# Kernel tuning notes

Measured on AMD Instinct MI355X. Metric: run time of the kernel, lower is better.

The kernel has to match this reference:

```python
import jax, jax.numpy as jnp
import numpy as np

NEG_SLOPE = 0.1
BN_EPS = 1e-5

def lrelu(z):
    return jax.nn.leaky_relu(z, NEG_SLOPE)

def conv1d(x, w, b):
    # x: [B,C,L], w: [O,I,K], 'same' padding for K=3
    y = jax.lax.conv_general_dilated(x, w, (1,), [(1, 1)], dimension_numbers=('NCH', 'OIH', 'NCH'))
    return y + b[None, :, None]

def batchnorm_train(x, g, be):
    # training-mode BatchNorm1d over (B, L) per channel; x: [B,C,L]
    m = x.mean(axis=(0, 2), keepdims=True)
    v = x.var(axis=(0, 2), keepdims=True)
    return g[None, :, None] * (x - m) * jax.lax.rsqrt(v + BN_EPS) + be[None, :, None]

def setup_inputs() -> dict:
    key = jax.random.key(0)
    ks = jax.random.split(key, 16)
    L, B, E = 100, 32, 512
    F, K, M, H, DEC = 256, 3, 128, 512, 512
    D = F + 2  # cnn feats + 2 coord dims
    s = 0.02
    inp = {
        'x': jax.random.normal(ks[0], (L, B, E), jnp.float32),
        'h': jax.random.normal(ks[1], (B, H), jnp.float32),
        'cw1': jax.random.normal(ks[2], (F, E, K), jnp.float32) * s,
        'cb1': jnp.zeros((F,), jnp.float32),
        'g1': jnp.ones((F,), jnp.float32), 'be1': jnp.zeros((F,), jnp.float32),
        'cw2': jax.random.normal(ks[3], (F, F, K), jnp.float32) * s,
        'cb2': jnp.zeros((F,), jnp.float32),
        'g2': jnp.ones((F,), jnp.float32), 'be2': jnp.zeros((F,), jnp.float32),
        'cw3': jax.random.normal(ks[4], (F, F, K), jnp.float32) * s,
        'cb3': jnp.zeros((F,), jnp.float32),
        'g3': jnp.ones((F,), jnp.float32), 'be3': jnp.zeros((F,), jnp.float32),
        'cw4': jax.random.normal(ks[5], (F, F, K), jnp.float32) * s,
        'cb4': jnp.zeros((F,), jnp.float32),
        'g4': jnp.ones((F,), jnp.float32), 'be4': jnp.zeros((F,), jnp.float32),
        'W1': jax.random.normal(ks[6], (2 * D + H, M), jnp.float32) * s,
        'b1': jnp.zeros((M,), jnp.float32),
        'W2': jax.random.normal(ks[7], (M, M), jnp.float32) * s,
        'b2': jnp.zeros((M,), jnp.float32),
        'W3': jax.random.normal(ks[8], (M, M), jnp.float32) * s,
        'b3': jnp.zeros((M,), jnp.float32),
        'W4': jax.random.normal(ks[9], (M, M), jnp.float32) * s,
        'b4': jnp.zeros((M,), jnp.float32),
        'F1': jax.random.normal(ks[10], (M, M), jnp.float32) * s,
        'fb1': jnp.zeros((M,), jnp.float32),
        'F2': jax.random.normal(ks[11], (M, DEC), jnp.float32) * s,
        'fb2': jnp.zeros((DEC,), jnp.float32),
    }
    return inp

def reference(x, h, cw1, cb1, g1, be1, cw2, cb2, g2, be2, cw3, cb3, g3, be3,
              cw4, cb4, g4, be4, W1, b1, W2, b2, W3, b3, W4, b4, F1, fb1, F2, fb2):
    # x: [L,B,E] -> [B,E,L]
    xc = jnp.transpose(x, (1, 2, 0))
    for cw, cb, g, be in ((cw1, cb1, g1, be1), (cw2, cb2, g2, be2),
                          (cw3, cb3, g3, be3), (cw4, cb4, g4, be4)):
        xc = batchnorm_train(lrelu(conv1d(xc, cw, cb)), g, be)
    xc = jnp.transpose(xc, (0, 2, 1))  # [B,L,F]
    B, L, _ = xc.shape
    # coordinate tensor: cvt_coord(i, L) = [(i/sqrt(L)-2)/2, (i%sqrt(L)-2)/2]
    i = jnp.arange(L, dtype=jnp.float32)
    sL = jnp.sqrt(jnp.float32(L))
    coord = jnp.stack([(i / sL - 2.0) / 2.0, (jnp.mod(i, sL) - 2.0) / 2.0], axis=-1)
    xf = jnp.concatenate([xc, jnp.broadcast_to(coord, (B, L, 2))], axis=-1)  # [B,L,D]
    D = xf.shape[-1]
    # pair[b,i,j] = [xf[b,j], xf[b,i], h[b]]; split W1 to avoid materializing concat
    Wa, Wb, Wc = W1[:D], W1[D:2 * D], W1[2 * D:]
    A = xf @ Wa                              # contribution of x_j, [B,L,M]
    C = xf @ Wb + (h @ Wc + b1)[:, None, :]  # contribution of x_i and h, [B,L,M]
    g = lrelu(C[:, :, None, :] + A[:, None, :, :])  # [B,L,L,M]
    g = lrelu(g @ W2 + b2)
    g = lrelu(g @ W3 + b3)
    g = lrelu(g @ W4 + b4)
    s = g.sum(axis=(1, 2))  # sum-pool over all L*L pairs -> [B,M]
    out = lrelu(lrelu(s @ F1 + fb1) @ F2 + fb2)  # [B,dec_hid]
    return out
```

## Files before the change

kernel.cpp:

```cpp
#include <hip/hip_runtime.h>
#include <hip/hip_bf16.h>
#include <stdint.h>
#include <stddef.h>

#define NEG 0.1f

typedef __attribute__((ext_vector_type(8))) short short8;
typedef __attribute__((ext_vector_type(16))) float floatx16;

__device__ __forceinline__ unsigned f2bf(float f) {
  union { float f; unsigned u; } v; v.f = f;
  unsigned r = v.u + 0x7FFFu + ((v.u >> 16) & 1u);
  return r >> 16;
}
__device__ __forceinline__ unsigned pk2bf(float a, float b) {
  __hip_bfloat162 hh = __float22bfloat162_rn(make_float2(a, b));
  union { __hip_bfloat162 h; unsigned u; } v; v.h = hh; return v.u;
}
__device__ __forceinline__ float bits2f(unsigned u) {
  union { unsigned u; float f; } v; v.u = u; return v.f;
}

__global__ void k_prep(const float* __restrict__ cw1, const float* __restrict__ cw2,
                       const float* __restrict__ cw3, const float* __restrict__ cw4,
                       unsigned short* __restrict__ wt1, unsigned short* __restrict__ wt2,
                       unsigned short* __restrict__ wt3, unsigned short* __restrict__ wt4,
                       const float* __restrict__ W1, unsigned short* __restrict__ wab,
                       const float* __restrict__ W2, const float* __restrict__ W3,
                       const float* __restrict__ W4, unsigned short* __restrict__ wmlp,
                       const float* __restrict__ h, float* __restrict__ hc) {
  __shared__ float tile[64 * 65];
  int bid = blockIdx.x, tid = threadIdx.x;
  if (bid < 1280) {
    int z = bid;
    int E; const float* cw; unsigned short* wt;
    if (z < 512) { E = 512; cw = cw1; wt = wt1; }
    else {
      int q = (z - 512) >> 8; E = 256;
      cw = (q == 0) ? cw2 : ((q == 1) ? cw3 : cw4);
      wt = (q == 0) ? wt2 : ((q == 1) ? wt3 : wt4);
      z = (z - 512) & 255;
    }
    int idx = z * 256 + tid;
    int f = idx / E, e = idx - f * E;
    const float* s = cw + (size_t)idx * 3;
    unsigned short* d = wt + (size_t)f * 3 * E + e;
    d[0] = (unsigned short)f2bf(s[0]);
    d[E] = (unsigned short)f2bf(s[1]);
    d[2 * E] = (unsigned short)f2bf(s[2]);
  } else if (bid < 1304) {
    int tw = bid - 1280;
    int half = tw / 12, rem = tw % 12, dt = rem >> 1, nt = rem & 1;
    int c = tid & 63, rq = tid >> 6;
#pragma unroll
    for (int it = 0; it < 16; ++it) {
      int r = rq + it * 4;
      int kp = dt * 64 + r;
      float v = 0.f;
      if (kp < 258) v = W1[(size_t)(half * 258 + kp) * 128 + nt * 64 + c];
      tile[r * 65 + c] = v;
    }
    __syncthreads();
#pragma unroll
    for (int it = 0; it < 16; ++it) {
      int r2 = rq + it * 4;
      wab[(size_t)(half * 128 + nt * 64 + r2) * 384 + dt * 64 + c] =
          (unsigned short)f2bf(tile[c * 65 + r2]);
    }
  } else if (bid < 1496) {
    int i2 = (bid - 1304) * 256 + tid;
    int n = i2 & 127, k = (i2 >> 7) & 127, zz = i2 >> 14;
    const float* W = (zz == 0) ? W2 : ((zz == 1) ? W3 : W4);
    float v = W[k * 128 + n];
    int w = n >> 5, l = ((k >> 3) & 1) * 32 + (n & 31), kk = k >> 4, j = k & 7;
    int i = (((zz * 4 + w) * 8 + kk) << 9) | (l << 3) | j;
    wmlp[i] = (unsigned short)f2bf(v);
  } else {
    int t = bid - 1496;
    int b = t >> 2, seg = t & 3;
    int m = tid & 127, sub = tid >> 7;
    int k0 = seg * 128 + sub * 64;
    const float* hr = h + b * 512 + k0;
    const float* Wc = W1 + (size_t)(516 + k0) * 128 + m;
    float a0 = 0.f, a1 = 0.f, a2 = 0.f, a3 = 0.f, a4 = 0.f, a5 = 0.f, a6 = 0.f, a7 = 0.f;
#pragma unroll
    for (int k = 0; k < 64; k += 8) {
      a0 += hr[k + 0] * Wc[(size_t)(k + 0) * 128];
      a1 += hr[k + 1] * Wc[(size_t)(k + 1) * 128];
      a2 += hr[k + 2] * Wc[(size_t)(k + 2) * 128];
      a3 += hr[k + 3] * Wc[(size_t)(k + 3) * 128];
      a4 += hr[k + 4] * Wc[(size_t)(k + 4) * 128];
      a5 += hr[k + 5] * Wc[(size_t)(k + 5) * 128];
      a6 += hr[k + 6] * Wc[(size_t)(k + 6) * 128];
      a7 += hr[k + 7] * Wc[(size_t)(k + 7) * 128];
    }
    float s = ((a0 + a1) + (a2 + a3)) + ((a4 + a5) + (a6 + a7));
    atomicAdd(&hc[b * 128 + m], s);
  }
}

__global__ __launch_bounds__(256, 2) void k_conv(
    const float* __restrict__ zin, const float* __restrict__ bnin,
    const float* __restrict__ gamv, const float* __restrict__ betv,
    const unsigned short* __restrict__ wt, const float* __restrict__ cb,
    float* __restrict__ zout, float* __restrict__ bnout, int E, int xmode) {
  extern __shared__ unsigned short smem[];
  const int SL = (E == 512) ? 520 : 264;
  unsigned short* slab = smem;
  unsigned short* Bs = smem + 34 * SL;
  const int K = 3 * E, NC = K >> 6, NCH = NC >> 1;
  const int esh = (E == 512) ? 9 : 8;
  int tid = threadIdx.x;
  int lane = tid & 63, wave = tid >> 6;
  int khalf = wave >> 1, cwave = wave & 1;
  int r0 = blockIdx.x * 32, ct = blockIdx.y;
  int i32 = lane & 31;
  int koff = (lane >> 5) << 3;

  int lrow = (r0 + i32) % 100;
  bool vks0 = (lrow >= 1), vks2 = (lrow <= 98);

  if (xmode) {
    for (int s = wave; s < 34; s += 4) {
      int m = r0 - 1 + s; m = min(max(m, 0), 3199);
      int b = m / 100, l = m - b * 100;
      size_t base = (size_t)(l * 32 + b) * 512;
#pragma unroll
      for (int cc = 0; cc < 2; ++cc) {
        int ch = cc * 256 + lane * 4;
        float4 v = *(const float4*)(zin + base + ch);
        uint2 p; p.x = pk2bf(v.x, v.y); p.y = pk2bf(v.z, v.w);
        *(uint2*)(&slab[s * SL + ch]) = p;
      }
    }
  } else {
    const float inv = 1.f / 3200.f;
    float sc[4], sh[4];
#pragma unroll
    for (int q = 0; q < 4; ++q) {
      int ch = lane * 4 + q;
      float mme = bnin[ch] * inv;
      float var = bnin[256 + ch] * inv - mme * mme;
      sc[q] = gamv[ch] * rsqrtf(var + 1e-5f);
      sh[q] = betv[ch] - mme * sc[q];
    }
    for (int s = wave; s < 34; s += 4) {
      int m = r0 - 1 + s; m = min(max(m, 0), 3199);
      float4 v = *(const float4*)(zin + (size_t)m * 256 + lane * 4);
      uint2 p;
      p.x = pk2bf(v.x * sc[0] + sh[0], v.y * sc[1] + sh[1]);
      p.y = pk2bf(v.z * sc[2] + sh[2], v.w * sc[3] + sh[3]);
      *(uint2*)(&slab[s * SL + lane * 4]) = p;
    }
  }

  floatx16 acc;
#pragma unroll
  for (int q = 0; q < 16; ++q) acc[q] = 0.f;

  int t128 = tid & 127;
  int brow = t128 >> 1, bhalf = (t128 & 1) * 32;
  const unsigned short* wrow = wt + (size_t)(ct * 64 + brow) * K + khalf * NCH * 64 + bhalf;
  uint4 pre[4];
#pragma unroll
  for (int t = 0; t < 4; ++t) pre[t] = *(const uint4*)(wrow + t * 8);

  for (int c = 0; c < NCH; ++c) {
    unsigned short* Bc = Bs + (khalf * 2 + (c & 1)) * (64 * 72);
#pragma unroll
    for (int t = 0; t < 4; ++t)
      *(uint4*)(&Bc[brow * 72 + bhalf + t * 8]) = pre[t];
    __syncthreads();
    if (c + 1 < NCH) {
#pragma unroll
      for (int t = 0; t < 4; ++t)
        pre[t] = *(const uint4*)(wrow + (c + 1) * 64 + t * 8);
    }
    int cg = khalf * NCH + c;
    int ks = (cg << 6) >> esh;
    int ebase = (cg << 6) & (E - 1);
    bool v = (ks == 0) ? vks0 : ((ks == 2) ? vks2 : true);
    int srow = i32 + ks;
#pragma unroll
    for (int kk = 0; kk < 4; ++kk) {
      short8 a = {};
      if (v) a = *(const short8*)(&slab[srow * SL + ebase + kk * 16 + koff]);
      short8 b8 = *(const short8*)(&Bc[(cwave * 32 + i32) * 72 + kk * 16 + koff]);
      acc = __builtin_amdgcn_mfma_f32_32x32x16_bf16(a, b8, acc, 0, 0, 0);
    }
  }

  __syncthreads();
  float* scr = (float*)smem;
  if (khalf == 1) {
#pragma unroll
    for (int reg = 0; reg < 16; ++reg) {
      int rowp = (reg & 3) + 8 * (reg >> 2) + 4 * (lane >> 5);
      scr[cwave * 1024 + rowp * 32 + i32] = acc[reg];
    }
  }
  __syncthreads();
  if (khalf == 0) {
    int f = ct * 64 + cwave * 32 + i32;
    float bias = cb[f];
    float s1 = 0.f, s2 = 0.f;
#pragma unroll
    for (int reg = 0; reg < 16; ++reg) {
      int rowp = (reg & 3) + 8 * (reg >> 2) + 4 * (lane >> 5);
      int m = r0 + rowp;
      float v = acc[reg] + scr[cwave * 1024 + rowp * 32 + i32] + bias;
      v = fmaxf(v, NEG * v);
      zout[(size_t)m * 256 + f] = v;
      s1 += v; s2 += v * v;
    }
    s1 += __shfl_xor(s1, 32, 64);
    s2 += __shfl_xor(s2, 32, 64);
    if (lane < 32) { atomicAdd(&bnout[f], s1); atomicAdd(&bnout[256 + f], s2); }
  }
}

__global__ __launch_bounds__(128, 2) void k_ac(
    const float* __restrict__ zin, const float* __restrict__ bnin,
    const float* __restrict__ gamv, const float* __restrict__ betv,
    const unsigned short* __restrict__ wab, const float* __restrict__ hc,
    const float* __restrict__ b1v,
    unsigned short* __restrict__ Abf, unsigned short* __restrict__ Cbf) {
  __shared__ unsigned short slab[32 * 328];
  __shared__ unsigned short Bs[2 * 64 * 72];
  int tid = threadIdx.x;
  int lane = tid & 63, wave = tid >> 6;
  int r0 = blockIdx.x * 32, ct = blockIdx.y;
  int i32 = lane & 31;
  int koff = (lane >> 5) << 3;
  const float inv = 1.f / 3200.f;

  {
    float sc[4], sh[4];
#pragma unroll
    for (int q = 0; q < 4; ++q) {
      int ch = lane * 4 + q;
      float mme = bnin[ch] * inv;
      float var = bnin[256 + ch] * inv - mme * mme;
      sc[q] = gamv[ch] * rsqrtf(var + 1e-5f);
      sh[q] = betv[ch] - mme * sc[q];
    }
    for (int s = wave; s < 32; s += 2) {
      int m = r0 + s;
      float4 v = *(const float4*)(zin + (size_t)m * 256 + lane * 4);
      uint2 p;
      p.x = pk2bf(v.x * sc[0] + sh[0], v.y * sc[1] + sh[1]);
      p.y = pk2bf(v.z * sc[2] + sh[2], v.w * sc[3] + sh[3]);
      *(uint2*)(&slab[s * 328 + lane * 4]) = p;
    }
    if (wave == 0) {
      int s = i32, half = (lane >> 5) * 32;
      int m = r0 + s, l = m % 100;
      float c0 = ((float)l * 0.1f - 2.0f) * 0.5f;
      float c1 = ((float)(l % 10) - 2.0f) * 0.5f;
#pragma unroll
      for (int seg = 0; seg < 4; ++seg) {
        uint4 z4; z4.x = z4.y = z4.z = z4.w = 0u;
        if (half == 0 && seg == 0) z4.x = pk2bf(c0, c1);
        *(uint4*)(&slab[s * 328 + 256 + half + seg * 8]) = z4;
      }
    }
  }

  floatx16 acc;
#pragma unroll
  for (int q = 0; q < 16; ++q) acc[q] = 0.f;

  int brow = tid >> 1, bhalf = (tid & 1) * 32;
  uint4 pre[4];
#pragma unroll
  for (int t = 0; t < 4; ++t)
    pre[t] = *(const uint4*)(wab + (size_t)(ct * 64 + brow) * 384 + bhalf + t * 8);

  for (int c = 0; c < 5; ++c) {
    unsigned short* Bc = Bs + (c & 1) * (64 * 72);
#pragma unroll
    for (int t = 0; t < 4; ++t)
      *(uint4*)(&Bc[brow * 72 + bhalf + t * 8]) = pre[t];
    __syncthreads();
    if (c + 1 < 5) {
#pragma unroll
      for (int t = 0; t < 4; ++t)
        pre[t] = *(const uint4*)(wab + (size_t)(ct * 64 + brow) * 384 + (c + 1) * 64 + bhalf + t * 8);
    }
#pragma unroll
    for (int kk = 0; kk < 4; ++kk) {
      short8 a = *(const short8*)(&slab[i32 * 328 + c * 64 + kk * 16 + koff]);
      short8 b8 = *(const short8*)(&Bc[(wave * 32 + i32) * 72 + kk * 16 + koff]);
      acc = __builtin_amdgcn_mfma_f32_32x32x16_bf16(a, b8, acc, 0, 0, 0);
    }
  }

  int n = ct * 64 + wave * 32 + i32;
#pragma unroll
  for (int reg = 0; reg < 16; ++reg) {
    int rowp = (reg & 3) + 8 * (reg >> 2) + 4 * (lane >> 5);
    int m = r0 + rowp;
    float v = acc[reg];
    if (ct < 2) {
      Abf[(size_t)m * 128 + n] = (unsigned short)f2bf(v);
    } else {
      int b = m / 100;
      int nc = n - 128;
      Cbf[(size_t)m * 128 + nc] =
          (unsigned short)f2bf(v + hc[b * 128 + nc] + b1v[nc]);
    }
  }
}

__device__ __forceinline__ void mlp_layer(const int z, const unsigned short* wlds,
                                          const float* bias_lds, const int lane,
                                          const int h, const short8 (&gin)[8],
                                          short8 (&gout)[8]) {
#pragma unroll
  for (int a = 0; a < 4; ++a) {
    floatx16 acc;
#pragma unroll
    for (int q = 0; q < 16; ++q) acc[q] = 0.f;
#pragma unroll
    for (int kk = 0; kk < 8; ++kk) {
      short8 wf = *(const short8*)(wlds + (((z * 4 + a) * 8 + kk) << 9) + lane * 8);
      acc = __builtin_amdgcn_mfma_f32_32x32x16_bf16(wf, gin[kk], acc, 0, 0, 0);
    }
#pragma unroll
    for (int qg = 0; qg < 4; ++qg) {
      float4 bb = *(const float4*)(bias_lds + z * 128 + a * 32 + qg * 8 + h * 4);
      float v0 = acc[qg * 4 + 0] + bb.x;
      float v1 = acc[qg * 4 + 1] + bb.y;
      float v2 = acc[qg * 4 + 2] + bb.z;
      float v3 = acc[qg * 4 + 3] + bb.w;
      acc[qg * 4 + 0] = fmaxf(v0, NEG * v0);
      acc[qg * 4 + 1] = fmaxf(v1, NEG * v1);
      acc[qg * 4 + 2] = fmaxf(v2, NEG * v2);
      acc[qg * 4 + 3] = fmaxf(v3, NEG * v3);
    }
#pragma unroll
    for (int c = 0; c < 2; ++c) {
      unsigned X0 = pk2bf(acc[8 * c + 0], acc[8 * c + 1]);
      unsigned X1 = pk2bf(acc[8 * c + 2], acc[8 * c + 3]);
      unsigned Y0 = pk2bf(acc[8 * c + 4], acc[8 * c + 5]);
      unsigned Y1 = pk2bf(acc[8 * c + 6], acc[8 * c + 7]);
      auto p0 = __builtin_amdgcn_permlane32_swap(X0, Y0, false, false);
      auto p1 = __builtin_amdgcn_permlane32_swap(X1, Y1, false, false);
      union { unsigned w[4]; short8 s; } uu;
      uu.w[0] = (unsigned)p0[0]; uu.w[1] = (unsigned)p1[0];
      uu.w[2] = (unsigned)p0[1]; uu.w[3] = (unsigned)p1[1];
      gout[2 * a + c] = uu.s;
    }
  }
}

__global__ __launch_bounds__(1024, 4) void k_mlp(
    const unsigned short* __restrict__ Abf, const unsigned short* __restrict__ Cbf,
    const unsigned short* __restrict__ wmlp, const float* __restrict__ b2,
    const float* __restrict__ b3, const float* __restrict__ b4,
    float* __restrict__ sout) {
  extern __shared__ unsigned short wsm[];
  float* bias_lds = (float*)(wsm + 49152);
  int tid = threadIdx.x, lane = tid & 63, wave = tid >> 6;
  int ln31 = lane & 31, h = lane >> 5;

  {
    const uint4* s4 = (const uint4*)wmlp;
    uint4* d4 = (uint4*)wsm;
#pragma unroll
    for (int i = 0; i < 6; ++i) d4[tid + i * 1024] = s4[tid + i * 1024];
    if (tid < 256) bias_lds[tid] = (tid < 128) ? b2[tid] : b3[tid - 128];
  }
  float b4v[4];
#pragma unroll
  for (int a = 0; a < 4; ++a) b4v[a] = b4[a * 32 + ln31];
  __syncthreads();

  int slot = blockIdx.x * 16 + wave;
  for (int it = 0; it < 3; ++it) {
    int u = it * 4096 + slot;
    if (u >= 10016) break;
    int b = u / 313, lu = u - b * 313;
    int r = lu * 32 + ln31;
    int rc = min(r, 9999);
    int i = rc / 100, j = rc - i * 100;
    const unsigned short* Crow = Cbf + (size_t)(b * 100 + i) * 128 + h * 8;
    const unsigned short* Arow = Abf + (size_t)(b * 100 + j) * 128 + h * 8;

    short8 ga[8], gb[8];
#pragma unroll
    for (int kk = 0; kk < 8; ++kk) {
      uint4 c4 = *(const uint4*)(Crow + kk * 16);
      uint4 a4 = *(const uint4*)(Arow + kk * 16);
      unsigned cw[4] = {c4.x, c4.y, c4.z, c4.w};
      unsigned aw[4] = {a4.x, a4.y, a4.z, a4.w};
      unsigned ow[4];
#pragma unroll
      for (int q = 0; q < 4; ++q) {
        float x0 = bits2f(cw[q] << 16) + bits2f(aw[q] << 16);
        float x1 = bits2f(cw[q] & 0xFFFF0000u) + bits2f(aw[q] & 0xFFFF0000u);
        x0 = fmaxf(x0, NEG * x0);
        x1 = fmaxf(x1, NEG * x1);
        ow[q] = pk2bf(x0, x1);
      }
      union { unsigned w[4]; short8 s; } uu;
      uu.w[0] = ow[0]; uu.w[1] = ow[1]; uu.w[2] = ow[2]; uu.w[3] = ow[3];
      ga[kk] = uu.s;
    }

    mlp_layer(0, wsm, bias_lds, lane, h, ga, gb);
    mlp_layer(1, wsm, bias_lds, lane, h, gb, ga);

#pragma unroll
    for (int a = 0; a < 4; ++a) {
      floatx16 acc;
#pragma unroll
      for (int q = 0; q < 16; ++q) acc[q] = 0.f;
#pragma unroll
      for (int kk = 0; kk < 8; ++kk) {
        short8 wf = *(const short8*)(wsm + (((8 + a) * 8 + kk) << 9) + lane * 8);
        acc = __builtin_amdgcn_mfma_f32_32x32x16_bf16(ga[kk], wf, acc, 0, 0, 0);
      }
      float s = 0.f;
#pragma unroll
      for (int reg = 0; reg < 16; ++reg) {
        int rowp = (reg & 3) + 8 * (reg >> 2) + 4 * h;
        float v = acc[reg] + b4v[a];
        v = fmaxf(v, NEG * v);
        s += (lu * 32 + rowp < 10000) ? v : 0.f;
      }
      s += __shfl_xor(s, 32, 64);
      if (lane < 32) atomicAdd(&sout[b * 128 + a * 32 + ln31], s);
    }
  }
}

__global__ void k_final(const float* __restrict__ s, const float* __restrict__ F1,
                        const float* __restrict__ fb1, const float* __restrict__ F2,
                        const float* __restrict__ fb2, float* __restrict__ out) {
  __shared__ float sl[128], t1[128];
  int b = blockIdx.x, t = threadIdx.x;
  if (t < 128) sl[t] = s[b * 128 + t];
  __syncthreads();
  if (t < 128) {
    float a = fb1[t];
    for (int k = 0; k < 128; ++k) a += sl[k] * F1[k * 128 + t];
    t1[t] = fmaxf(a, NEG * a);
  }
  __syncthreads();
  for (int o = t; o < 512; o += 256) {
    float a = fb2[o];
    for (int k = 0; k < 128; ++k) a += t1[k] * F2[k * 512 + o];
    out[b * 512 + o] = fmaxf(a, NEG * a);
  }
}

extern "C" void kernel_launch(void* const* d_in, const int* in_sizes, int n_in,
                              void* d_out, int out_size, void* d_ws, size_t ws_size,
                              hipStream_t stream) {
  const float* x   = (const float*)d_in[0];
  const float* h   = (const float*)d_in[1];
  const float* cw1 = (const float*)d_in[2];
  const float* cb1 = (const float*)d_in[3];
  const float* g1  = (const float*)d_in[4];
  const float* be1 = (const float*)d_in[5];
  const float* cw2 = (const float*)d_in[6];
  const float* cb2 = (const float*)d_in[7];
  const float* g2  = (const float*)d_in[8];
  const float* be2 = (const float*)d_in[9];
  const float* cw3 = (const float*)d_in[10];
  const float* cb3 = (const float*)d_in[11];
  const float* g3  = (const float*)d_in[12];
  const float* be3 = (const float*)d_in[13];
  const float* cw4 = (const float*)d_in[14];
  const float* cb4 = (const float*)d_in[15];
  const float* g4  = (const float*)d_in[16];
  const float* be4 = (const float*)d_in[17];
  const float* W1  = (const float*)d_in[18];
  const float* b1  = (const float*)d_in[19];
  const float* W2  = (const float*)d_in[20];
  const float* b2  = (const float*)d_in[21];
  const float* W3  = (const float*)d_in[22];
  const float* b3  = (const float*)d_in[23];
  const float* W4  = (const float*)d_in[24];
  const float* b4  = (const float*)d_in[25];
  const float* F1  = (const float*)d_in[26];
  const float* fb1 = (const float*)d_in[27];
  const float* F2  = (const float*)d_in[28];
  const float* fb2 = (const float*)d_in[29];

  char* ws = (char*)d_ws;
  float* bn0  = (float*)(ws + 0);
  float* bn1  = (float*)(ws + 2048);
  float* bn2  = (float*)(ws + 4096);
  float* bn3  = (float*)(ws + 6144);
  float* sbuf = (float*)(ws + 8192);
  float* hc   = (float*)(ws + 24576);
  float* za   = (float*)(ws + 40960);
  float* zb   = (float*)(ws + 3317760);
  unsigned short* wt1  = (unsigned short*)(ws + 6594560);
  unsigned short* wt2  = (unsigned short*)(ws + 7380992);
  unsigned short* wt3  = (unsigned short*)(ws + 7774208);
  unsigned short* wt4  = (unsigned short*)(ws + 8167424);
  unsigned short* wab  = (unsigned short*)(ws + 8560640);
  unsigned short* wmlp = (unsigned short*)(ws + 8757248);
  unsigned short* Abf  = (unsigned short*)(ws + 8855552);
  unsigned short* Cbf  = (unsigned short*)(ws + 9674752);

  hipMemsetAsync(d_ws, 0, 40960, stream);

  k_prep<<<1624, 256, 0, stream>>>(cw1, cw2, cw3, cw4, wt1, wt2, wt3, wt4,
                                   W1, wab, W2, W3, W4, wmlp, h, hc);

  const int lds1 = (34 * 520 + 4 * 64 * 72) * 2;
  const int lds2 = (34 * 264 + 4 * 64 * 72) * 2;
  k_conv<<<dim3(100, 4), 256, lds1, stream>>>(x,  nullptr, nullptr, nullptr, wt1, cb1, za, bn0, 512, 1);
  k_conv<<<dim3(100, 4), 256, lds2, stream>>>(za, bn0, g1, be1, wt2, cb2, zb, bn1, 256, 0);
  k_conv<<<dim3(100, 4), 256, lds2, stream>>>(zb, bn1, g2, be2, wt3, cb3, za, bn2, 256, 0);
  k_conv<<<dim3(100, 4), 256, lds2, stream>>>(za, bn2, g3, be3, wt4, cb4, zb, bn3, 256, 0);

  k_ac<<<dim3(100, 4), 128, 0, stream>>>(zb, bn3, g4, be4, wab, hc, b1, Abf, Cbf);

  const int ldsm = 49152 * 2 + 256 * 4;
  k_mlp<<<256, 1024, ldsm, stream>>>(Abf, Cbf, wmlp, b2, b3, b4, sbuf);
  k_final<<<32, 256, 0, stream>>>(sbuf, F1, fb1, F2, fb2, (float*)d_out);
}
```

Before: 280.8 us.

## Pre-swizzle conv weights into MFMA fragment layout and split K across waves

Conv and A/C projection weights are now stored during prep in MFMA-fragment order, so each wave loads B operands straight from global memory without staging them through LDS. The conv and k_ac kernels switch to 32-column tiles with K split four ways across waves and a reduction through LDS, doubling the grid and raising occupancy. Other changes: the memset is folded into the prep kernel, the hc atomics become a block reduction, biases seed the MLP accumulators, and the pair-pooling kernel skips row masking except on the tail tile. The K-split adds an LDS reduction, and weights are now read uncached by each block.

```diff
diff --git a/kernel.cpp b/kernel.cpp
--- a/kernel.cpp
+++ b/kernel.cpp
@@ -21,15 +21,17 @@
   union { unsigned u; float f; } v; v.u = u; return v.f;
 }
 
+
 __global__ void k_prep(const float* __restrict__ cw1, const float* __restrict__ cw2,
                        const float* __restrict__ cw3, const float* __restrict__ cw4,
                        unsigned short* __restrict__ wt1, unsigned short* __restrict__ wt2,
                        unsigned short* __restrict__ wt3, unsigned short* __restrict__ wt4,
-                       const float* __restrict__ W1, unsigned short* __restrict__ wab,
+                       const float* __restrict__ W1, unsigned short* __restrict__ wabf,
                        const float* __restrict__ W2, const float* __restrict__ W3,
                        const float* __restrict__ W4, unsigned short* __restrict__ wmlp,
-                       const float* __restrict__ h, float* __restrict__ hc) {
-  __shared__ float tile[64 * 65];
+                       const float* __restrict__ h, float* __restrict__ hc,
+                       float* __restrict__ zmem) {
+  __shared__ float tile[256];
   int bid = blockIdx.x, tid = threadIdx.x;
   if (bid < 1280) {
     int z = bid;
@@ -41,31 +43,34 @@
       wt = (q == 0) ? wt2 : ((q == 1) ? wt3 : wt4);
       z = (z - 512) & 255;
     }
+    int NCw = (3 * E) >> 6;
     int idx = z * 256 + tid;
     int f = idx / E, e = idx - f * E;
     const float* s = cw + (size_t)idx * 3;
-    unsigned short* d = wt + (size_t)f * 3 * E + e;
-    d[0] = (unsigned short)f2bf(s[0]);
-    d[E] = (unsigned short)f2bf(s[1]);
-    d[2 * E] = (unsigned short)f2bf(s[2]);
+    int ct = f >> 5, i32 = f & 31;
+#pragma unroll
+    for (int ks = 0; ks < 3; ++ks) {
+      int kcol = ks * E + e;
+      int cg = kcol >> 6, kk = (kcol >> 4) & 3, hh = (kcol >> 3) & 1, j = kcol & 7;
+      wt[(size_t)((((ct * NCw + cg) * 4 + kk) * 2 + hh) * 32 + i32) * 8 + j] =
+          (unsigned short)f2bf(s[ks]);
+    }
   } else if (bid < 1304) {
     int tw = bid - 1280;
     int half = tw / 12, rem = tw % 12, dt = rem >> 1, nt = rem & 1;
     int c = tid & 63, rq = tid >> 6;
-#pragma unroll
-    for (int it = 0; it < 16; ++it) {
-      int r = rq + it * 4;
-      int kp = dt * 64 + r;
-      float v = 0.f;
-      if (kp < 258) v = W1[(size_t)(half * 258 + kp) * 128 + nt * 64 + c];
-      tile[r * 65 + c] = v;
-    }
-    __syncthreads();
+    int n = half * 128 + nt * 64 + c;
+    int ct = n >> 5, i32 = n & 31;
 #pragma unroll
     for (int it = 0; it < 16; ++it) {
       int r2 = rq + it * 4;
-      wab[(size_t)(half * 128 + nt * 64 + r2) * 384 + dt * 64 + c] =
-          (unsigned short)f2bf(tile[c * 65 + r2]);
+      int kp = dt * 64 + r2;
+      if (kp < 320) {
+        float v = (kp < 258) ? W1[(size_t)(half * 258 + kp) * 128 + nt * 64 + c] : 0.f;
+        int cg = kp >> 6, kk = (kp >> 4) & 3, hh = (kp >> 3) & 1, j = kp & 7;
+        wabf[(size_t)((((ct * 5 + cg) * 4 + kk) * 2 + hh) * 32 + i32) * 8 + j] =
+            (unsigned short)f2bf(v);
+      }
     }
   } else if (bid < 1496) {
     int i2 = (bid - 1304) * 256 + tid;
@@ -75,16 +80,14 @@
     int w = n >> 5, l = ((k >> 3) & 1) * 32 + (n & 31), kk = k >> 4, j = k & 7;
     int i = (((zz * 4 + w) * 8 + kk) << 9) | (l << 3) | j;
     wmlp[i] = (unsigned short)f2bf(v);
-  } else {
-    int t = bid - 1496;
-    int b = t >> 2, seg = t & 3;
-    int m = tid & 127, sub = tid >> 7;
-    int k0 = seg * 128 + sub * 64;
-    const float* hr = h + b * 512 + k0;
-    const float* Wc = W1 + (size_t)(516 + k0) * 128 + m;
+  } else if (bid < 1528) {
+    int b = bid - 1496;
+    int m = tid & 127, kh = tid >> 7;
+    const float* hr = h + b * 512 + kh * 256;
+    const float* Wc = W1 + (size_t)(516 + kh * 256) * 128 + m;
     float a0 = 0.f, a1 = 0.f, a2 = 0.f, a3 = 0.f, a4 = 0.f, a5 = 0.f, a6 = 0.f, a7 = 0.f;
 #pragma unroll
-    for (int k = 0; k < 64; k += 8) {
+    for (int k = 0; k < 256; k += 8) {
       a0 += hr[k + 0] * Wc[(size_t)(k + 0) * 128];
       a1 += hr[k + 1] * Wc[(size_t)(k + 1) * 128];
       a2 += hr[k + 2] * Wc[(size_t)(k + 2) * 128];
@@ -95,27 +98,30 @@
       a7 += hr[k + 7] * Wc[(size_t)(k + 7) * 128];
     }
     float s = ((a0 + a1) + (a2 + a3)) + ((a4 + a5) + (a6 + a7));
-    atomicAdd(&hc[b * 128 + m], s);
-  }
-}
-
-__global__ __launch_bounds__(256, 2) void k_conv(
+    tile[tid] = s;
+    __syncthreads();
+    if (kh == 0) hc[b * 128 + m] = tile[m] + tile[128 + m];
+  } else {
+    int i = (bid - 1528) * 256 + tid;
+    zmem[i] = 0.f;
+  }
+}
+
+__global__ __launch_bounds__(256, 4) void k_conv(
     const float* __restrict__ zin, const float* __restrict__ bnin,
     const float* __restrict__ gamv, const float* __restrict__ betv,
-    const unsigned short* __restrict__ wt, const float* __restrict__ cb,
+    const unsigned short* __restrict__ wtf, const float* __restrict__ cb,
     float* __restrict__ zout, float* __restrict__ bnout, int E, int xmode) {
   extern __shared__ unsigned short smem[];
   const int SL = (E == 512) ? 520 : 264;
   unsigned short* slab = smem;
-  unsigned short* Bs = smem + 34 * SL;
-  const int K = 3 * E, NC = K >> 6, NCH = NC >> 1;
+  const int NC = (3 * E) >> 6, NCQ = NC >> 2;
   const int esh = (E == 512) ? 9 : 8;
   int tid = threadIdx.x;
   int lane = tid & 63, wave = tid >> 6;
-  int khalf = wave >> 1, cwave = wave & 1;
-  int r0 = blockIdx.x * 32, ct = blockIdx.y;
-  int i32 = lane & 31;
-  int koff = (lane >> 5) << 3;
+  int bid = blockIdx.x;
+  int r0 = (bid % 100) * 32, ct = bid / 100;
+  int i32 = lane & 31, h = lane >> 5;
 
   int lrow = (r0 + i32) % 100;
   bool vks0 = (lrow >= 1), vks2 = (lrow <= 98);
@@ -153,30 +159,28 @@
       *(uint2*)(&slab[s * SL + lane * 4]) = p;
     }
   }
+  __syncthreads();
 
   floatx16 acc;
 #pragma unroll
   for (int q = 0; q < 16; ++q) acc[q] = 0.f;
 
-  int t128 = tid & 127;
-  int brow = t128 >> 1, bhalf = (t128 & 1) * 32;
-  const unsigned short* wrow = wt + (size_t)(ct * 64 + brow) * K + khalf * NCH * 64 + bhalf;
-  uint4 pre[4];
-#pragma unroll
-  for (int t = 0; t < 4; ++t) pre[t] = *(const uint4*)(wrow + t * 8);
-
-  for (int c = 0; c < NCH; ++c) {
-    unsigned short* Bc = Bs + (khalf * 2 + (c & 1)) * (64 * 72);
-#pragma unroll
-    for (int t = 0; t < 4; ++t)
-      *(uint4*)(&Bc[brow * 72 + bhalf + t * 8]) = pre[t];
-    __syncthreads();
-    if (c + 1 < NCH) {
-#pragma unroll
-      for (int t = 0; t < 4; ++t)
-        pre[t] = *(const uint4*)(wrow + (c + 1) * 64 + t * 8);
-    }
-    int cg = khalf * NCH + c;
+  int cg0 = wave * NCQ;
+  const unsigned short* wp = wtf + (size_t)((ct * NC + cg0) * 8 + h) * 256 + i32 * 8;
+  short8 bpre[4];
+#pragma unroll
+  for (int kk = 0; kk < 4; ++kk) bpre[kk] = *(const short8*)(wp + kk * 512);
+
+  for (int c = 0; c < NCQ; ++c) {
+    short8 bcur[4];
+#pragma unroll
+    for (int kk = 0; kk < 4; ++kk) bcur[kk] = bpre[kk];
+    if (c + 1 < NCQ) {
+      wp += 2048;
+#pragma unroll
+      for (int kk = 0; kk < 4; ++kk) bpre[kk] = *(const short8*)(wp + kk * 512);
+    }
+    int cg = cg0 + c;
     int ks = (cg << 6) >> esh;
     int ebase = (cg << 6) & (E - 1);
     bool v = (ks == 0) ? vks0 : ((ks == 2) ? vks2 : true);
@@ -184,31 +188,31 @@
 #pragma unroll
     for (int kk = 0; kk < 4; ++kk) {
       short8 a = {};
-      if (v) a = *(const short8*)(&slab[srow * SL + ebase + kk * 16 + koff]);
-      short8 b8 = *(const short8*)(&Bc[(cwave * 32 + i32) * 72 + kk * 16 + koff]);
-      acc = __builtin_amdgcn_mfma_f32_32x32x16_bf16(a, b8, acc, 0, 0, 0);
+      if (v) a = *(const short8*)(&slab[srow * SL + ebase + kk * 16 + h * 8]);
+      acc = __builtin_amdgcn_mfma_f32_32x32x16_bf16(a, bcur[kk], acc, 0, 0, 0);
     }
   }
 
   __syncthreads();
   float* scr = (float*)smem;
-  if (khalf == 1) {
+  if (wave) {
 #pragma unroll
     for (int reg = 0; reg < 16; ++reg) {
-      int rowp = (reg & 3) + 8 * (reg >> 2) + 4 * (lane >> 5);
-      scr[cwave * 1024 + rowp * 32 + i32] = acc[reg];
-    }
-  }
-  __syncthreads();
-  if (khalf == 0) {
-    int f = ct * 64 + cwave * 32 + i32;
+      int rowp = (reg & 3) + 8 * (reg >> 2) + 4 * h;
+      scr[(wave - 1) * 1024 + rowp * 32 + i32] = acc[reg];
+    }
+  }
+  __syncthreads();
+  if (wave == 0) {
+    int f = ct * 32 + i32;
     float bias = cb[f];
     float s1 = 0.f, s2 = 0.f;
 #pragma unroll
     for (int reg = 0; reg < 16; ++reg) {
-      int rowp = (reg & 3) + 8 * (reg >> 2) + 4 * (lane >> 5);
+      int rowp = (reg & 3) + 8 * (reg >> 2) + 4 * h;
       int m = r0 + rowp;
-      float v = acc[reg] + scr[cwave * 1024 + rowp * 32 + i32] + bias;
+      float v = acc[reg] + scr[rowp * 32 + i32] + scr[1024 + rowp * 32 + i32]
+              + scr[2048 + rowp * 32 + i32] + bias;
       v = fmaxf(v, NEG * v);
       zout[(size_t)m * 256 + f] = v;
       s1 += v; s2 += v * v;
@@ -219,19 +223,19 @@
   }
 }
 
-__global__ __launch_bounds__(128, 2) void k_ac(
+__global__ __launch_bounds__(256, 4) void k_ac(
     const float* __restrict__ zin, const float* __restrict__ bnin,
     const float* __restrict__ gamv, const float* __restrict__ betv,
-    const unsigned short* __restrict__ wab, const float* __restrict__ hc,
+    const unsigned short* __restrict__ wabf, const float* __restrict__ hc,
     const float* __restrict__ b1v,
     unsigned short* __restrict__ Abf, unsigned short* __restrict__ Cbf) {
-  __shared__ unsigned short slab[32 * 328];
-  __shared__ unsigned short Bs[2 * 64 * 72];
+  extern __shared__ unsigned short smem[];
+  unsigned short* slab = smem;
   int tid = threadIdx.x;
   int lane = tid & 63, wave = tid >> 6;
-  int r0 = blockIdx.x * 32, ct = blockIdx.y;
-  int i32 = lane & 31;
-  int koff = (lane >> 5) << 3;
+  int bid = blockIdx.x;
+  int r0 = (bid % 100) * 32, ct = bid / 100;
+  int i32 = lane & 31, h = lane >> 5;
   const float inv = 1.f / 3200.f;
 
   {
@@ -244,7 +248,7 @@
       sc[q] = gamv[ch] * rsqrtf(var + 1e-5f);
       sh[q] = betv[ch] - mme * sc[q];
     }
-    for (int s = wave; s < 32; s += 2) {
+    for (int s = wave; s < 32; s += 4) {
       int m = r0 + s;
       float4 v = *(const float4*)(zin + (size_t)m * 256 + lane * 4);
       uint2 p;
@@ -253,7 +257,7 @@
       *(uint2*)(&slab[s * 328 + lane * 4]) = p;
     }
     if (wave == 0) {
-      int s = i32, half = (lane >> 5) * 32;
+      int s = i32, half = h * 32;
       int m = r0 + s, l = m % 100;
       float c0 = ((float)l * 0.1f - 2.0f) * 0.5f;
       float c1 = ((float)(l % 10) - 2.0f) * 0.5f;
@@ -265,49 +269,52 @@
       }
     }
   }
+  __syncthreads();
 
   floatx16 acc;
 #pragma unroll
   for (int q = 0; q < 16; ++q) acc[q] = 0.f;
 
-  int brow = tid >> 1, bhalf = (tid & 1) * 32;
-  uint4 pre[4];
-#pragma unroll
-  for (int t = 0; t < 4; ++t)
-    pre[t] = *(const uint4*)(wab + (size_t)(ct * 64 + brow) * 384 + bhalf + t * 8);
-
-  for (int c = 0; c < 5; ++c) {
-    unsigned short* Bc = Bs + (c & 1) * (64 * 72);
-#pragma unroll
-    for (int t = 0; t < 4; ++t)
-      *(uint4*)(&Bc[brow * 72 + bhalf + t * 8]) = pre[t];
-    __syncthreads();
-    if (c + 1 < 5) {
-#pragma unroll
-      for (int t = 0; t < 4; ++t)
-        pre[t] = *(const uint4*)(wab + (size_t)(ct * 64 + brow) * 384 + (c + 1) * 64 + bhalf + t * 8);
-    }
-#pragma unroll
-    for (int kk = 0; kk < 4; ++kk) {
-      short8 a = *(const short8*)(&slab[i32 * 328 + c * 64 + kk * 16 + koff]);
-      short8 b8 = *(const short8*)(&Bc[(wave * 32 + i32) * 72 + kk * 16 + koff]);
-      acc = __builtin_amdgcn_mfma_f32_32x32x16_bf16(a, b8, acc, 0, 0, 0);
-    }
-  }
-
-  int n = ct * 64 + wave * 32 + i32;
-#pragma unroll
-  for (int reg = 0; reg < 16; ++reg) {
-    int rowp = (reg & 3) + 8 * (reg >> 2) + 4 * (lane >> 5);
-    int m = r0 + rowp;
-    float v = acc[reg];
-    if (ct < 2) {
-      Abf[(size_t)m * 128 + n] = (unsigned short)f2bf(v);
-    } else {
-      int b = m / 100;
-      int nc = n - 128;
-      Cbf[(size_t)m * 128 + nc] =
-          (unsigned short)f2bf(v + hc[b * 128 + nc] + b1v[nc]);
+#pragma unroll
+  for (int cc = 0; cc < 2; ++cc) {
+    int cg = wave + cc * 4;
+    if (cg <= 4) {
+      const unsigned short* wp = wabf + (size_t)((ct * 5 + cg) * 8 + h) * 256 + i32 * 8;
+#pragma unroll
+      for (int kk = 0; kk < 4; ++kk) {
+        short8 a = *(const short8*)(&slab[i32 * 328 + cg * 64 + kk * 16 + h * 8]);
+        short8 b8 = *(const short8*)(wp + kk * 512);
+        acc = __builtin_amdgcn_mfma_f32_32x32x16_bf16(a, b8, acc, 0, 0, 0);
+      }
+    }
+  }
+
+  __syncthreads();
+  float* scr = (float*)smem;
+  if (wave) {
+#pragma unroll
+    for (int reg = 0; reg < 16; ++reg) {
+      int rowp = (reg & 3) + 8 * (reg >> 2) + 4 * h;
+      scr[(wave - 1) * 1024 + rowp * 32 + i32] = acc[reg];
+    }
+  }
+  __syncthreads();
+  if (wave == 0) {
+    int n = ct * 32 + i32;
+#pragma unroll
+    for (int reg = 0; reg < 16; ++reg) {
+      int rowp = (reg & 3) + 8 * (reg >> 2) + 4 * h;
+      int m = r0 + rowp;
+      float v = acc[reg] + scr[rowp * 32 + i32] + scr[1024 + rowp * 32 + i32]
+              + scr[2048 + rowp * 32 + i32];
+      if (ct < 4) {
+        Abf[(size_t)m * 128 + n] = (unsigned short)f2bf(v);
+      } else {
+        int b = m / 100;
+        int nc = n - 128;
+        Cbf[(size_t)m * 128 + nc] =
+            (unsigned short)f2bf(v + hc[b * 128 + nc] + b1v[nc]);
+      }
     }
   }
 }
@@ -320,23 +327,20 @@
   for (int a = 0; a < 4; ++a) {
     floatx16 acc;
 #pragma unroll
-    for (int q = 0; q < 16; ++q) acc[q] = 0.f;
+    for (int qg = 0; qg < 4; ++qg) {
+      float4 bb = *(const float4*)(bias_lds + z * 128 + a * 32 + qg * 8 + h * 4);
+      acc[qg * 4 + 0] = bb.x; acc[qg * 4 + 1] = bb.y;
+      acc[qg * 4 + 2] = bb.z; acc[qg * 4 + 3] = bb.w;
+    }
 #pragma unroll
     for (int kk = 0; kk < 8; ++kk) {
       short8 wf = *(const short8*)(wlds + (((z * 4 + a) * 8 + kk) << 9) + lane * 8);
       acc = __builtin_amdgcn_mfma_f32_32x32x16_bf16(wf, gin[kk], acc, 0, 0, 0);
     }
 #pragma unroll
-    for (int qg = 0; qg < 4; ++qg) {
-      float4 bb = *(const float4*)(bias_lds + z * 128 + a * 32 + qg * 8 + h * 4);
-      float v0 = acc[qg * 4 + 0] + bb.x;
-      float v1 = acc[qg * 4 + 1] + bb.y;
-      float v2 = acc[qg * 4 + 2] + bb.z;
-      float v3 = acc[qg * 4 + 3] + bb.w;
-      acc[qg * 4 + 0] = fmaxf(v0, NEG * v0);
-      acc[qg * 4 + 1] = fmaxf(v1, NEG * v1);
-      acc[qg * 4 + 2] = fmaxf(v2, NEG * v2);
-      acc[qg * 4 + 3] = fmaxf(v3, NEG * v3);
+    for (int q = 0; q < 16; ++q) {
+      float v = acc[q];
+      acc[q] = fmaxf(v, NEG * v);
     }
 #pragma unroll
     for (int c = 0; c < 2; ++c) {
@@ -381,8 +385,9 @@
     int u = it * 4096 + slot;
     if (u >= 10016) break;
     int b = u / 313, lu = u - b * 313;
+    bool tail = (lu == 312);
     int r = lu * 32 + ln31;
-    int rc = min(r, 9999);
+    int rc = tail ? min(r, 9999) : r;
     int i = rc / 100, j = rc - i * 100;
     const unsigned short* Crow = Cbf + (size_t)(b * 100 + i) * 128 + h * 8;
     const unsigned short* Arow = Abf + (size_t)(b * 100 + j) * 128 + h * 8;
@@ -414,20 +419,29 @@
 #pragma unroll
     for (int a = 0; a < 4; ++a) {
       floatx16 acc;
-#pragma unroll
-      for (int q = 0; q < 16; ++q) acc[q] = 0.f;
+      float binit = b4v[a];
+#pragma unroll
+      for (int q = 0; q < 16; ++q) acc[q] = binit;
 #pragma unroll
       for (int kk = 0; kk < 8; ++kk) {
         short8 wf = *(const short8*)(wsm + (((8 + a) * 8 + kk) << 9) + lane * 8);
         acc = __builtin_amdgcn_mfma_f32_32x32x16_bf16(ga[kk], wf, acc, 0, 0, 0);
       }
       float s = 0.f;
-#pragma unroll
-      for (int reg = 0; reg < 16; ++reg) {
-        int rowp = (reg & 3) + 8 * (reg >> 2) + 4 * h;
-        float v = acc[reg] + b4v[a];
-        v = fmaxf(v, NEG * v);
-        s += (lu * 32 + rowp < 10000) ? v : 0.f;
+      if (!tail) {
+#pragma unroll
+        for (int reg = 0; reg < 16; ++reg) {
+          float v = acc[reg];
+          s += fmaxf(v, NEG * v);
+        }
+      } else {
+#pragma unroll
+        for (int reg = 0; reg < 16; ++reg) {
+          int rowp = (reg & 3) + 8 * (reg >> 2) + 4 * h;
+          float v = acc[reg];
+          v = fmaxf(v, NEG * v);
+          s += (lu * 32 + rowp < 10000) ? v : 0.f;
+        }
       }
       s += __shfl_xor(s, 32, 64);
       if (lane < 32) atomicAdd(&sout[b * 128 + a * 32 + ln31], s);
@@ -490,6 +504,7 @@
   const float* fb2 = (const float*)d_in[29];
 
   char* ws = (char*)d_ws;
+  float* zmem = (float*)(ws + 0);
   float* bn0  = (float*)(ws + 0);
   float* bn1  = (float*)(ws + 2048);
   float* bn2  = (float*)(ws + 4096);
@@ -502,24 +517,23 @@
   unsigned short* wt2  = (unsigned short*)(ws + 7380992);
   unsigned short* wt3  = (unsigned short*)(ws + 7774208);
   unsigned short* wt4  = (unsigned short*)(ws + 8167424);
-  unsigned short* wab  = (unsigned short*)(ws + 8560640);
+  unsigned short* wabf = (unsigned short*)(ws + 8560640);
   unsigned short* wmlp = (unsigned short*)(ws + 8757248);
   unsigned short* Abf  = (unsigned short*)(ws + 8855552);
   unsigned short* Cbf  = (unsigned short*)(ws + 9674752);
 
-  hipMemsetAsync(d_ws, 0, 40960, stream);
-
-  k_prep<<<1624, 256, 0, stream>>>(cw1, cw2, cw3, cw4, wt1, wt2, wt3, wt4,
-                                   W1, wab, W2, W3, W4, wmlp, h, hc);
-
-  const int lds1 = (34 * 520 + 4 * 64 * 72) * 2;
-  const int lds2 = (34 * 264 + 4 * 64 * 72) * 2;
-  k_conv<<<dim3(100, 4), 256, lds1, stream>>>(x,  nullptr, nullptr, nullptr, wt1, cb1, za, bn0, 512, 1);
-  k_conv<<<dim3(100, 4), 256, lds2, stream>>>(za, bn0, g1, be1, wt2, cb2, zb, bn1, 256, 0);
-  k_conv<<<dim3(100, 4), 256, lds2, stream>>>(zb, bn1, g2, be2, wt3, cb3, za, bn2, 256, 0);
-  k_conv<<<dim3(100, 4), 256, lds2, stream>>>(za, bn2, g3, be3, wt4, cb4, zb, bn3, 256, 0);
-
-  k_ac<<<dim3(100, 4), 128, 0, stream>>>(zb, bn3, g4, be4, wab, hc, b1, Abf, Cbf);
+  k_prep<<<1552, 256, 0, stream>>>(cw1, cw2, cw3, cw4, wt1, wt2, wt3, wt4,
+                                   W1, wabf, W2, W3, W4, wmlp, h, hc, zmem);
+
+  const int lds1 = 34 * 520 * 2;
+  const int lds2 = 34 * 264 * 2;
+  k_conv<<<800, 256, lds1, stream>>>(x,  nullptr, nullptr, nullptr, wt1, cb1, za, bn0, 512, 1);
+  k_conv<<<800, 256, lds2, stream>>>(za, bn0, g1, be1, wt2, cb2, zb, bn1, 256, 0);
+  k_conv<<<800, 256, lds2, stream>>>(zb, bn1, g2, be2, wt3, cb3, za, bn2, 256, 0);
+  k_conv<<<800, 256, lds2, stream>>>(za, bn2, g3, be3, wt4, cb4, zb, bn3, 256, 0);
+
+  const int ldsa = 32 * 328 * 2;
+  k_ac<<<800, 256, ldsa, stream>>>(zb, bn3, g4, be4, wabf, hc, b1, Abf, Cbf);
 
   const int ldsm = 49152 * 2 + 256 * 4;
   k_mlp<<<256, 1024, ldsm, stream>>>(Abf, Cbf, wmlp, b2, b3, b4, sbuf);
```

Result: faster. 258.5 us (-7.9%).
